# Kernel optimization log

Hardware: AMD Instinct MI355X
Metric: run time of the kernel (lower is better)

Reference implementation:

```python
import jax, jax.numpy as jnp
import numpy as np
import math

D_MODEL = 1024
NUM_HEADS = 16
D_K = D_MODEL // NUM_HEADS
B, T = 2, 2048


def setup_inputs() -> dict:
    key = jax.random.key(0)
    ks = jax.random.split(key, 9)
    s = 1.0 / math.sqrt(D_MODEL)
    inp = {
        'x': jax.random.normal(ks[0], (B, T, D_MODEL), dtype=jnp.float32),
        'mask': jnp.tril(jnp.ones((1, 1, T, T), dtype=jnp.int32)),
        'Wq': jax.random.uniform(ks[1], (D_MODEL, D_MODEL), jnp.float32, -s, s),
        'bq': jax.random.uniform(ks[2], (D_MODEL,), jnp.float32, -s, s),
        'Wk': jax.random.uniform(ks[3], (D_MODEL, D_MODEL), jnp.float32, -s, s),
        'bk': jax.random.uniform(ks[4], (D_MODEL,), jnp.float32, -s, s),
        'Wv': jax.random.uniform(ks[5], (D_MODEL, D_MODEL), jnp.float32, -s, s),
        'bv': jax.random.uniform(ks[6], (D_MODEL,), jnp.float32, -s, s),
        'Wo': jax.random.uniform(ks[7], (D_MODEL, D_MODEL), jnp.float32, -s, s),
        'bo': jax.random.uniform(ks[8], (D_MODEL,), jnp.float32, -s, s),
    }
    return inp


def reference(x, mask, Wq, bq, Wk, bk, Wv, bv, Wo, bo):
    Bsz, Tlen, C = x.shape
    # projections; torch Linear computes x @ W.T + b, here W stored as (in,out)-like square so use x @ W + b with W meaning W.T
    q = (x @ Wq + bq).reshape(Bsz, Tlen, NUM_HEADS, D_K).transpose(0, 2, 1, 3)
    k = (x @ Wk + bk).reshape(Bsz, Tlen, NUM_HEADS, D_K).transpose(0, 2, 1, 3)
    v = (x @ Wv + bv).reshape(Bsz, Tlen, NUM_HEADS, D_K).transpose(0, 2, 1, 3)
    scores = jnp.einsum('bhqd,bhkd->bhqk', q, k) / math.sqrt(D_K)  # (B,H,T,T)
    scores = jnp.where(mask == 0, -jnp.inf, scores)
    attn = jax.nn.softmax(scores, axis=-1)
    out = jnp.einsum('bhqk,bhkd->bhqd', attn, v)
    out = out.transpose(0, 2, 1, 3).reshape(Bsz, Tlen, C)
    return out @ Wo + bo
```

## Files before the change

kernel.cpp:

```cpp
#include <hip/hip_runtime.h>
#include <math.h>

typedef unsigned short ushort_t;
typedef short short8 __attribute__((ext_vector_type(8)));
typedef float f32x4 __attribute__((ext_vector_type(4)));

#define DMODEL 1024
#define NHEADS 16
#define DKH    64
#define BATCH  2
#define SEQ    2048
#define BT     (BATCH * SEQ)

__device__ __forceinline__ ushort_t f2bf(float f) {
    union { float f; unsigned u; } a; a.f = f;
    return (ushort_t)((a.u + 0x7FFFu + ((a.u >> 16) & 1u)) >> 16);
}

__device__ __forceinline__ void async_copy16(const ushort_t* g, ushort_t* l) {
    __builtin_amdgcn_global_load_lds(
        (__attribute__((address_space(1))) void*)g,
        (__attribute__((address_space(3))) void*)l, 16, 0, 0);
}

__global__ __launch_bounds__(256) void prep_kernel(
    const float* __restrict__ x, ushort_t* __restrict__ xb,
    const float* __restrict__ Wq, const float* __restrict__ Wk,
    const float* __restrict__ Wv, const float* __restrict__ Wo,
    ushort_t* __restrict__ WqT, ushort_t* __restrict__ WkT,
    ushort_t* __restrict__ WvT, ushort_t* __restrict__ WoT)
{
    __shared__ ushort_t tile[64][72];
    const int bx = blockIdx.x;
    const int tid = threadIdx.x;

    if (bx < 2048) {
        size_t i = ((size_t)bx * 256 + tid) * 8;
        float4 a = *(const float4*)(x + i);
        float4 b = *(const float4*)(x + i + 4);
        union { ushort_t u[8]; short8 v; } r;
        r.u[0] = f2bf(a.x); r.u[1] = f2bf(a.y); r.u[2] = f2bf(a.z); r.u[3] = f2bf(a.w);
        r.u[4] = f2bf(b.x); r.u[5] = f2bf(b.y); r.u[6] = f2bf(b.z); r.u[7] = f2bf(b.w);
        *(short8*)(xb + i) = r.v;
        return;
    }

    const int idx = bx - 2048;
    const int z  = idx >> 8;
    const int n0 = ((idx >> 4) & 15) * 64;
    const int k0 = (idx & 15) * 64;
    const float* W = (z == 0) ? Wq : (z == 1) ? Wk : (z == 2) ? Wv : Wo;
    ushort_t*   WT = (z == 0) ? WqT : (z == 1) ? WkT : (z == 2) ? WvT : WoT;

    const int r  = tid >> 2;
    const int cb = (tid & 3) * 16;
#pragma unroll
    for (int u = 0; u < 4; ++u) {
        float4 v = *(const float4*)(W + (size_t)(k0 + r) * DMODEL + n0 + cb + u * 4);
        union { ushort_t u4[4]; unsigned long long ll; } p;
        p.u4[0] = f2bf(v.x); p.u4[1] = f2bf(v.y); p.u4[2] = f2bf(v.z); p.u4[3] = f2bf(v.w);
        *(unsigned long long*)&tile[r][cb + u * 4] = p.ll;
    }
    __syncthreads();
    const int n  = tid >> 2;
    const int kb = (tid & 3) * 16;
#pragma unroll
    for (int half = 0; half < 2; ++half) {
        union { ushort_t u8[8]; short8 v; } p;
#pragma unroll
        for (int j = 0; j < 8; ++j) p.u8[j] = tile[kb + half * 8 + j][n];
        *(short8*)(WT + (size_t)(n0 + n) * DMODEL + k0 + kb + half * 8) = p.v;
    }
}

__device__ __forceinline__ void gemm_dbuf_128(
    const ushort_t* __restrict__ A, const ushort_t* __restrict__ B,
    int m0, int n0, ushort_t* At, ushort_t* Bt, f32x4 (&acc)[4][4])
{
    const int tid  = threadIdx.x;
    const int w    = tid >> 6, lane = tid & 63;
    const int l15  = lane & 15, quad = lane >> 4;
    const int wm   = w >> 1, wn = w & 1;
    const int srow = lane >> 3;
    const int scol = ((lane & 7) ^ srow) << 3;
    const int swz  = l15 & 7;

#pragma unroll
    for (int c = 0; c < 4; ++c) {
        int ch = w * 4 + c;
        async_copy16(A + (size_t)(m0 + ch * 8 + srow) * DMODEL + scol, At + ch * 512);
        async_copy16(B + (size_t)(n0 + ch * 8 + srow) * DMODEL + scol, Bt + ch * 512);
    }
    __syncthreads();

    for (int kt = 0; kt < DMODEL / 64; ++kt) {
        const int cur = (kt & 1) << 13;
        if (kt + 1 < DMODEL / 64) {
            const int nxt = cur ^ 8192;
            const int k0 = (kt + 1) * 64;
#pragma unroll
            for (int c = 0; c < 4; ++c) {
                int ch = w * 4 + c;
                async_copy16(A + (size_t)(m0 + ch * 8 + srow) * DMODEL + k0 + scol,
                             At + nxt + ch * 512);
                async_copy16(B + (size_t)(n0 + ch * 8 + srow) * DMODEL + k0 + scol,
                             Bt + nxt + ch * 512);
            }
        }
#pragma unroll
        for (int kk = 0; kk < 2; ++kk) {
            short8 af[4], bf[4];
#pragma unroll
            for (int t = 0; t < 4; ++t) {
                int ra = wm * 64 + t * 16 + l15;
                int rb = wn * 64 + t * 16 + l15;
                af[t] = *(const short8*)(At + cur + ra * 64 +
                                         (((kk * 4 + quad) ^ swz) << 3));
                bf[t] = *(const short8*)(Bt + cur + rb * 64 +
                                         (((kk * 4 + quad) ^ swz) << 3));
            }
#pragma unroll
            for (int mt = 0; mt < 4; ++mt)
#pragma unroll
                for (int nt = 0; nt < 4; ++nt)
                    acc[mt][nt] = __builtin_amdgcn_mfma_f32_16x16x32_bf16(
                        af[mt], bf[nt], acc[mt][nt], 0, 0, 0);
        }
        __syncthreads();
    }
}

__device__ __forceinline__ void gemm_dbuf_m64(
    const ushort_t* __restrict__ A, const ushort_t* __restrict__ B,
    int m0, int n0, ushort_t* At, ushort_t* Bt, f32x4 (&acc)[2][4])
{
    const int tid  = threadIdx.x;
    const int w    = tid >> 6, lane = tid & 63;
    const int l15  = lane & 15, quad = lane >> 4;
    const int wm   = w & 1, wn = w >> 1;
    const int srow = lane >> 3;
    const int scol = ((lane & 7) ^ srow) << 3;
    const int swz  = l15 & 7;

#pragma unroll
    for (int c = 0; c < 2; ++c) {
        int ch = w * 2 + c;
        async_copy16(A + (size_t)(m0 + ch * 8 + srow) * DMODEL + scol, At + ch * 512);
    }
#pragma unroll
    for (int c = 0; c < 4; ++c) {
        int ch = w * 4 + c;
        async_copy16(B + (size_t)(n0 + ch * 8 + srow) * DMODEL + scol, Bt + ch * 512);
    }
    __syncthreads();

    for (int kt = 0; kt < DMODEL / 64; ++kt) {
        const int curA = (kt & 1) << 12;
        const int curB = (kt & 1) << 13;
        if (kt + 1 < DMODEL / 64) {
            const int k0 = (kt + 1) * 64;
#pragma unroll
            for (int c = 0; c < 2; ++c) {
                int ch = w * 2 + c;
                async_copy16(A + (size_t)(m0 + ch * 8 + srow) * DMODEL + k0 + scol,
                             At + (curA ^ 4096) + ch * 512);
            }
#pragma unroll
            for (int c = 0; c < 4; ++c) {
                int ch = w * 4 + c;
                async_copy16(B + (size_t)(n0 + ch * 8 + srow) * DMODEL + k0 + scol,
                             Bt + (curB ^ 8192) + ch * 512);
            }
        }
#pragma unroll
        for (int kk = 0; kk < 2; ++kk) {
            short8 af[2], bf[4];
#pragma unroll
            for (int t = 0; t < 2; ++t) {
                int ra = wm * 32 + t * 16 + l15;
                af[t] = *(const short8*)(At + curA + ra * 64 +
                                         (((kk * 4 + quad) ^ swz) << 3));
            }
#pragma unroll
            for (int t = 0; t < 4; ++t) {
                int rb = wn * 64 + t * 16 + l15;
                bf[t] = *(const short8*)(Bt + curB + rb * 64 +
                                         (((kk * 4 + quad) ^ swz) << 3));
            }
#pragma unroll
            for (int mt = 0; mt < 2; ++mt)
#pragma unroll
                for (int nt = 0; nt < 4; ++nt)
                    acc[mt][nt] = __builtin_amdgcn_mfma_f32_16x16x32_bf16(
                        af[mt], bf[nt], acc[mt][nt], 0, 0, 0);
        }
        __syncthreads();
    }
}

__global__ __launch_bounds__(256) void qkv_gemm(
    const ushort_t* __restrict__ xb,
    const ushort_t* __restrict__ WqT, const ushort_t* __restrict__ WkT,
    const ushort_t* __restrict__ WvT,
    const float* __restrict__ bq, const float* __restrict__ bk,
    const float* __restrict__ bv,
    ushort_t* __restrict__ Qb, ushort_t* __restrict__ Kb, ushort_t* __restrict__ VTo)
{
    const int z = blockIdx.z;
    const ushort_t* WT = (z == 0) ? WqT : (z == 1) ? WkT : WvT;
    const float* bias  = (z == 0) ? bq : (z == 1) ? bk : bv;

    __shared__ ushort_t At[2 * 8192];
    __shared__ ushort_t Bt[2 * 8192];
    const int m0 = blockIdx.x * 128, n0 = blockIdx.y * 128;

    f32x4 zero = {0.f, 0.f, 0.f, 0.f};
    f32x4 acc[4][4];
#pragma unroll
    for (int i = 0; i < 4; ++i)
#pragma unroll
        for (int j = 0; j < 4; ++j) acc[i][j] = zero;

    gemm_dbuf_128(xb, WT, m0, n0, At, Bt, acc);

    const int tid = threadIdx.x, w = tid >> 6, lane = tid & 63;
    const int l15 = lane & 15, quad = lane >> 4;
    const int wm = w >> 1, wn = w & 1;

    float bcol[4];
#pragma unroll
    for (int nt = 0; nt < 4; ++nt) bcol[nt] = bias[n0 + wn * 64 + nt * 16 + l15];

    if (z == 2) {
#pragma unroll
        for (int mt = 0; mt < 4; ++mt) {
            int row0 = m0 + wm * 64 + mt * 16 + quad * 4;
            int b = row0 >> 11, t = row0 & (SEQ - 1);
            int tb = t & ~63;
            int idxp = ((mt & 1) << 2) | (quad << 3) | ((mt >> 1) << 5);
#pragma unroll
            for (int nt = 0; nt < 4; ++nt) {
                int col = n0 + wn * 64 + nt * 16 + l15;
                int h = col >> 6, d = col & 63;
                union { ushort_t u4[4]; unsigned long long ll; } pk;
#pragma unroll
                for (int reg = 0; reg < 4; ++reg)
                    pk.u4[reg] = f2bf(acc[mt][nt][reg] + bcol[nt]);
                *(unsigned long long*)(VTo +
                    ((size_t)(b * NHEADS + h) * DKH + d) * SEQ + tb + idxp) = pk.ll;
            }
        }
    } else {
        ushort_t* out = (z == 0) ? Qb : Kb;
#pragma unroll
        for (int mt = 0; mt < 4; ++mt)
#pragma unroll
            for (int reg = 0; reg < 4; ++reg) {
                int row = m0 + wm * 64 + mt * 16 + quad * 4 + reg;
                int b = row >> 11, t = row & (SEQ - 1);
#pragma unroll
                for (int nt = 0; nt < 4; ++nt) {
                    int col = n0 + wn * 64 + nt * 16 + l15;
                    int h = col >> 6, d = col & 63;
                    out[((((size_t)b * NHEADS + h) * SEQ + t) << 6) + d] =
                        f2bf(acc[mt][nt][reg] + bcol[nt]);
                }
            }
    }
}

__global__ __launch_bounds__(256) void attn_kernel(
    const ushort_t* __restrict__ Qb, const ushort_t* __restrict__ Kb,
    const ushort_t* __restrict__ VT, ushort_t* __restrict__ AO)
{
    const int bi = blockIdx.x;
    const int bh = bi & 31;
    const int b  = bh >> 4, h = bh & 15;
    const int qq = bi >> 5;
    const int tid = threadIdx.x, w = tid >> 6, lane = tid & 63;
    const int l15 = lane & 15, quad = lane >> 4;

    __shared__ ushort_t Kt[2][64 * 64];
    __shared__ ushort_t Vt[2][64 * 64];

    const ushort_t* Kbase = Kb + (((size_t)bh * SEQ) << 6);
    const ushort_t* Vbase = VT + (size_t)bh * DKH * SEQ;

    const int srow = lane >> 3;
    const int schx = (lane & 7) ^ srow;
    const int swz  = l15 & 7;
    const f32x4 zero = {0.f, 0.f, 0.f, 0.f};
    const float cexp = 0.18033688011112042f;

    union { ushort_t u8[8]; short8 v; } ones;
#pragma unroll
    for (int j = 0; j < 8; ++j) ones.u8[j] = 0x3F80;

    for (int job = 0; job < 2; ++job) {
        const int qt = job ? (31 - qq) : qq;
        const int q0 = qt * 64;
        const int nk = qt + 1;

        short8 qa[2];
#pragma unroll
        for (int ks = 0; ks < 2; ++ks)
            qa[ks] = *(const short8*)(
                Qb + (((size_t)bh * SEQ + q0 + w * 16 + l15) << 6) + ks * 32 + quad * 8);

        f32x4 lacc = zero;
        f32x4 o[4];
#pragma unroll
        for (int dt = 0; dt < 4; ++dt) o[dt] = zero;

#pragma unroll
        for (int c = 0; c < 2; ++c) {
            int chunk = w * 2 + c;
            async_copy16(Kbase + (((size_t)(chunk * 8 + srow)) << 6) + schx * 8,
                         &Kt[0][chunk * 512]);
            async_copy16(Vbase + (size_t)(chunk * 8 + srow) * SEQ + schx * 8,
                         &Vt[0][chunk * 512]);
        }
        __syncthreads();

        for (int kt = 0; kt < nk; ++kt) {
            const int buf = kt & 1;
            if (kt + 1 < nk) {
                const int kt0n = (kt + 1) * 64;
#pragma unroll
                for (int c = 0; c < 2; ++c) {
                    int chunk = w * 2 + c;
                    async_copy16(Kbase + (((size_t)(kt0n + chunk * 8 + srow)) << 6) + schx * 8,
                                 &Kt[buf ^ 1][chunk * 512]);
                    async_copy16(Vbase + (size_t)(chunk * 8 + srow) * SEQ + kt0n + schx * 8,
                                 &Vt[buf ^ 1][chunk * 512]);
                }
            }

            short8 kf[4][2], vf[2][4];
#pragma unroll
            for (int kt_i = 0; kt_i < 4; ++kt_i)
#pragma unroll
                for (int ks = 0; ks < 2; ++ks)
                    kf[kt_i][ks] = *(const short8*)&Kt[buf][(kt_i * 16 + l15) * 64 +
                                                            (((ks * 4 + quad) ^ swz) << 3)];
#pragma unroll
            for (int g = 0; g < 2; ++g)
#pragma unroll
                for (int dt = 0; dt < 4; ++dt)
                    vf[g][dt] = *(const short8*)&Vt[buf][(dt * 16 + l15) * 64 +
                                                         ((((g << 2) | quad) ^ swz) << 3)];

            f32x4 sc[4];
#pragma unroll
            for (int kt_i = 0; kt_i < 4; ++kt_i) sc[kt_i] = zero;
#pragma unroll
            for (int ks = 0; ks < 2; ++ks)
#pragma unroll
                for (int kt_i = 0; kt_i < 4; ++kt_i)
                    sc[kt_i] = __builtin_amdgcn_mfma_f32_16x16x32_bf16(
                        kf[kt_i][ks], qa[ks], sc[kt_i], 0, 0, 0);

            const bool domask = (kt == qt);
            const int qabs = q0 + w * 16 + l15;
            unsigned pka[4], pkb[4];
#pragma unroll
            for (int kt_i = 0; kt_i < 4; ++kt_i) {
                float p[4];
#pragma unroll
                for (int r = 0; r < 4; ++r) {
                    float pv = exp2f(cexp * sc[kt_i][r]);
                    if (domask && (kt * 64 + kt_i * 16 + quad * 4 + r) > qabs) pv = 0.f;
                    p[r] = pv;
                }
                pka[kt_i] = __builtin_amdgcn_perm(
                    __float_as_uint(p[1]), __float_as_uint(p[0]), 0x07060302u);
                pkb[kt_i] = __builtin_amdgcn_perm(
                    __float_as_uint(p[3]), __float_as_uint(p[2]), 0x07060302u);
            }

#pragma unroll
            for (int g = 0; g < 2; ++g) {
                union { unsigned u[4]; short8 v; } pf;
                pf.u[0] = pka[2 * g];
                pf.u[1] = pkb[2 * g];
                pf.u[2] = pka[2 * g + 1];
                pf.u[3] = pkb[2 * g + 1];
                lacc = __builtin_amdgcn_mfma_f32_16x16x32_bf16(
                    pf.v, ones.v, lacc, 0, 0, 0);
#pragma unroll
                for (int dt = 0; dt < 4; ++dt)
                    o[dt] = __builtin_amdgcn_mfma_f32_16x16x32_bf16(
                        pf.v, vf[g][dt], o[dt], 0, 0, 0);
            }

            __syncthreads();
        }

#pragma unroll
        for (int r = 0; r < 4; ++r) {
            float inv = 1.0f / lacc[r];
            int t = q0 + w * 16 + quad * 4 + r;
#pragma unroll
            for (int dt = 0; dt < 4; ++dt)
                AO[((size_t)b * SEQ + t) * DMODEL + h * 64 + dt * 16 + l15] =
                    f2bf(o[dt][r] * inv);
        }
    }
}

__global__ __launch_bounds__(256) void out_gemm(
    const ushort_t* __restrict__ AO, const ushort_t* __restrict__ WoT,
    const float* __restrict__ bo, float* __restrict__ out)
{
    __shared__ ushort_t At[2 * 4096];
    __shared__ ushort_t Bt[2 * 8192];
    const int m0 = blockIdx.x * 64, n0 = blockIdx.y * 128;

    f32x4 zero = {0.f, 0.f, 0.f, 0.f};
    f32x4 acc[2][4];
#pragma unroll
    for (int i = 0; i < 2; ++i)
#pragma unroll
        for (int j = 0; j < 4; ++j) acc[i][j] = zero;

    gemm_dbuf_m64(AO, WoT, m0, n0, At, Bt, acc);

    const int tid = threadIdx.x, w = tid >> 6, lane = tid & 63;
    const int l15 = lane & 15, quad = lane >> 4;
    const int wm = w & 1, wn = w >> 1;

    float bcol[4];
#pragma unroll
    for (int nt = 0; nt < 4; ++nt) bcol[nt] = bo[n0 + wn * 64 + nt * 16 + l15];

#pragma unroll
    for (int mt = 0; mt < 2; ++mt)
#pragma unroll
        for (int reg = 0; reg < 4; ++reg) {
            int row = m0 + wm * 32 + mt * 16 + quad * 4 + reg;
#pragma unroll
            for (int nt = 0; nt < 4; ++nt) {
                int col = n0 + wn * 64 + nt * 16 + l15;
                out[(size_t)row * DMODEL + col] = acc[mt][nt][reg] + bcol[nt];
            }
        }
}

extern "C" void kernel_launch(void* const* d_in, const int* in_sizes, int n_in,
                              void* d_out, int out_size, void* d_ws, size_t ws_size,
                              hipStream_t stream)
{
    const float* x  = (const float*)d_in[0];
    const float* Wq = (const float*)d_in[2];
    const float* bq = (const float*)d_in[3];
    const float* Wk = (const float*)d_in[4];
    const float* bk = (const float*)d_in[5];
    const float* Wv = (const float*)d_in[6];
    const float* bv = (const float*)d_in[7];
    const float* Wo = (const float*)d_in[8];
    const float* bo = (const float*)d_in[9];
    float* out = (float*)d_out;

    ushort_t* ws = (ushort_t*)d_ws;
    size_t off = 0;
    ushort_t* xb  = ws + off; off += (size_t)BT * DMODEL;
    ushort_t* WqT = ws + off; off += (size_t)DMODEL * DMODEL;
    ushort_t* WkT = ws + off; off += (size_t)DMODEL * DMODEL;
    ushort_t* WvT = ws + off; off += (size_t)DMODEL * DMODEL;
    ushort_t* WoT = ws + off; off += (size_t)DMODEL * DMODEL;
    ushort_t* Qb  = ws + off; off += (size_t)BT * DMODEL;
    ushort_t* Kb  = ws + off; off += (size_t)BT * DMODEL;
    ushort_t* VTb = ws + off; off += (size_t)BT * DMODEL;
    ushort_t* AOb = ws + off; off += (size_t)BT * DMODEL;

    prep_kernel<<<2048 + 1024, 256, 0, stream>>>(
        x, xb, Wq, Wk, Wv, Wo, WqT, WkT, WvT, WoT);
    qkv_gemm<<<dim3(BT / 128, DMODEL / 128, 3), 256, 0, stream>>>(
        xb, WqT, WkT, WvT, bq, bk, bv, Qb, Kb, VTb);
    attn_kernel<<<dim3(SEQ / 64 * NHEADS * BATCH / 2), 256, 0, stream>>>(
        Qb, Kb, VTb, AOb);
    out_gemm<<<dim3(BT / 64, DMODEL / 128), 256, 0, stream>>>(
        AOb, WoT, bo, out);
}
```

Baseline: 201.7 us.

## Halve GEMM K-tile to 32 with packed two-row swizzled LDS layout

Both projection GEMM helpers now stage 32-wide K slices instead of 64. Two rows are packed into each 64-element LDS line with a new XOR swizzle, and the shared buffers shrink accordingly. The goal is to cut LDS use per block so more blocks can reside on a CU and hide latency better. In exchange there are twice as many loop iterations and barriers, and each barrier covers less MFMA work.

```diff
diff --git a/kernel.cpp b/kernel.cpp
--- a/kernel.cpp
+++ b/kernel.cpp
@@ -81,51 +81,51 @@
     const int w    = tid >> 6, lane = tid & 63;
     const int l15  = lane & 15, quad = lane >> 4;
     const int wm   = w >> 1, wn = w & 1;
-    const int srow = lane >> 3;
-    const int scol = ((lane & 7) ^ srow) << 3;
-    const int swz  = l15 & 7;
-
-#pragma unroll
-    for (int c = 0; c < 4; ++c) {
-        int ch = w * 4 + c;
-        async_copy16(A + (size_t)(m0 + ch * 8 + srow) * DMODEL + scol, At + ch * 512);
-        async_copy16(B + (size_t)(n0 + ch * 8 + srow) * DMODEL + scol, Bt + ch * 512);
+    const int s    = (lane & 7) ^ ((lane >> 3) & 7);
+    const int rofs = ((lane >> 3) << 1) | (s >> 2);
+    const int cofs = (s & 3) << 3;
+
+    const ushort_t* Asrc = A + (size_t)m0 * DMODEL + cofs;
+    const ushort_t* Bsrc = B + (size_t)n0 * DMODEL + cofs;
+
+#pragma unroll
+    for (int c = 0; c < 2; ++c) {
+        int ch = w * 2 + c;
+        async_copy16(Asrc + (size_t)(ch * 16 + rofs) * DMODEL, At + ch * 512);
+        async_copy16(Bsrc + (size_t)(ch * 16 + rofs) * DMODEL, Bt + ch * 512);
     }
     __syncthreads();
 
-    for (int kt = 0; kt < DMODEL / 64; ++kt) {
-        const int cur = (kt & 1) << 13;
-        if (kt + 1 < DMODEL / 64) {
-            const int nxt = cur ^ 8192;
-            const int k0 = (kt + 1) * 64;
-#pragma unroll
-            for (int c = 0; c < 4; ++c) {
-                int ch = w * 4 + c;
-                async_copy16(A + (size_t)(m0 + ch * 8 + srow) * DMODEL + k0 + scol,
+    for (int kt = 0; kt < DMODEL / 32; ++kt) {
+        const int cur = (kt & 1) << 12;
+        if (kt + 1 < DMODEL / 32) {
+            const int nxt = cur ^ 4096;
+            const int k0 = (kt + 1) * 32;
+#pragma unroll
+            for (int c = 0; c < 2; ++c) {
+                int ch = w * 2 + c;
+                async_copy16(Asrc + (size_t)(ch * 16 + rofs) * DMODEL + k0,
                              At + nxt + ch * 512);
-                async_copy16(B + (size_t)(n0 + ch * 8 + srow) * DMODEL + k0 + scol,
+                async_copy16(Bsrc + (size_t)(ch * 16 + rofs) * DMODEL + k0,
                              Bt + nxt + ch * 512);
             }
         }
-#pragma unroll
-        for (int kk = 0; kk < 2; ++kk) {
-            short8 af[4], bf[4];
-#pragma unroll
-            for (int t = 0; t < 4; ++t) {
-                int ra = wm * 64 + t * 16 + l15;
-                int rb = wn * 64 + t * 16 + l15;
-                af[t] = *(const short8*)(At + cur + ra * 64 +
-                                         (((kk * 4 + quad) ^ swz) << 3));
-                bf[t] = *(const short8*)(Bt + cur + rb * 64 +
-                                         (((kk * 4 + quad) ^ swz) << 3));
-            }
-#pragma unroll
-            for (int mt = 0; mt < 4; ++mt)
-#pragma unroll
-                for (int nt = 0; nt < 4; ++nt)
-                    acc[mt][nt] = __builtin_amdgcn_mfma_f32_16x16x32_bf16(
-                        af[mt], bf[nt], acc[mt][nt], 0, 0, 0);
-        }
+        short8 af[4], bf[4];
+#pragma unroll
+        for (int t = 0; t < 4; ++t) {
+            int ra = wm * 64 + t * 16 + l15;
+            int rb = wn * 64 + t * 16 + l15;
+            af[t] = *(const short8*)(At + cur + (ra >> 1) * 64 +
+                     (((((ra & 1) << 2) | quad) ^ ((ra >> 1) & 7)) << 3));
+            bf[t] = *(const short8*)(Bt + cur + (rb >> 1) * 64 +
+                     (((((rb & 1) << 2) | quad) ^ ((rb >> 1) & 7)) << 3));
+        }
+#pragma unroll
+        for (int mt = 0; mt < 4; ++mt)
+#pragma unroll
+            for (int nt = 0; nt < 4; ++nt)
+                acc[mt][nt] = __builtin_amdgcn_mfma_f32_16x16x32_bf16(
+                    af[mt], bf[nt], acc[mt][nt], 0, 0, 0);
         __syncthreads();
     }
 }
@@ -138,62 +138,54 @@
     const int w    = tid >> 6, lane = tid & 63;
     const int l15  = lane & 15, quad = lane >> 4;
     const int wm   = w & 1, wn = w >> 1;
-    const int srow = lane >> 3;
-    const int scol = ((lane & 7) ^ srow) << 3;
-    const int swz  = l15 & 7;
-
+    const int s    = (lane & 7) ^ ((lane >> 3) & 7);
+    const int rofs = ((lane >> 3) << 1) | (s >> 2);
+    const int cofs = (s & 3) << 3;
+
+    const ushort_t* Asrc = A + (size_t)m0 * DMODEL + cofs;
+    const ushort_t* Bsrc = B + (size_t)n0 * DMODEL + cofs;
+
+    async_copy16(Asrc + (size_t)(w * 16 + rofs) * DMODEL, At + w * 512);
 #pragma unroll
     for (int c = 0; c < 2; ++c) {
         int ch = w * 2 + c;
-        async_copy16(A + (size_t)(m0 + ch * 8 + srow) * DMODEL + scol, At + ch * 512);
-    }
-#pragma unroll
-    for (int c = 0; c < 4; ++c) {
-        int ch = w * 4 + c;
-        async_copy16(B + (size_t)(n0 + ch * 8 + srow) * DMODEL + scol, Bt + ch * 512);
+        async_copy16(Bsrc + (size_t)(ch * 16 + rofs) * DMODEL, Bt + ch * 512);
     }
     __syncthreads();
 
-    for (int kt = 0; kt < DMODEL / 64; ++kt) {
-        const int curA = (kt & 1) << 12;
-        const int curB = (kt & 1) << 13;
-        if (kt + 1 < DMODEL / 64) {
-            const int k0 = (kt + 1) * 64;
+    for (int kt = 0; kt < DMODEL / 32; ++kt) {
+        const int curA = (kt & 1) << 11;
+        const int curB = (kt & 1) << 12;
+        if (kt + 1 < DMODEL / 32) {
+            const int k0 = (kt + 1) * 32;
+            async_copy16(Asrc + (size_t)(w * 16 + rofs) * DMODEL + k0,
+                         At + (curA ^ 2048) + w * 512);
 #pragma unroll
             for (int c = 0; c < 2; ++c) {
                 int ch = w * 2 + c;
-                async_copy16(A + (size_t)(m0 + ch * 8 + srow) * DMODEL + k0 + scol,
-                             At + (curA ^ 4096) + ch * 512);
-            }
-#pragma unroll
-            for (int c = 0; c < 4; ++c) {
-                int ch = w * 4 + c;
-                async_copy16(B + (size_t)(n0 + ch * 8 + srow) * DMODEL + k0 + scol,
-                             Bt + (curB ^ 8192) + ch * 512);
-            }
-        }
-#pragma unroll
-        for (int kk = 0; kk < 2; ++kk) {
-            short8 af[2], bf[4];
-#pragma unroll
-            for (int t = 0; t < 2; ++t) {
-                int ra = wm * 32 + t * 16 + l15;
-                af[t] = *(const short8*)(At + curA + ra * 64 +
-                                         (((kk * 4 + quad) ^ swz) << 3));
-            }
-#pragma unroll
-            for (int t = 0; t < 4; ++t) {
-                int rb = wn * 64 + t * 16 + l15;
-                bf[t] = *(const short8*)(Bt + curB + rb * 64 +
-                                         (((kk * 4 + quad) ^ swz) << 3));
-            }
-#pragma unroll
-            for (int mt = 0; mt < 2; ++mt)
-#pragma unroll
-                for (int nt = 0; nt < 4; ++nt)
-                    acc[mt][nt] = __builtin_amdgcn_mfma_f32_16x16x32_bf16(
-                        af[mt], bf[nt], acc[mt][nt], 0, 0, 0);
-        }
+                async_copy16(Bsrc + (size_t)(ch * 16 + rofs) * DMODEL + k0,
+                             Bt + (curB ^ 4096) + ch * 512);
+            }
+        }
+        short8 af[2], bf[4];
+#pragma unroll
+        for (int t = 0; t < 2; ++t) {
+            int ra = wm * 32 + t * 16 + l15;
+            af[t] = *(const short8*)(At + curA + (ra >> 1) * 64 +
+                     (((((ra & 1) << 2) | quad) ^ ((ra >> 1) & 7)) << 3));
+        }
+#pragma unroll
+        for (int t = 0; t < 4; ++t) {
+            int rb = wn * 64 + t * 16 + l15;
+            bf[t] = *(const short8*)(Bt + curB + (rb >> 1) * 64 +
+                     (((((rb & 1) << 2) | quad) ^ ((rb >> 1) & 7)) << 3));
+        }
+#pragma unroll
+        for (int mt = 0; mt < 2; ++mt)
+#pragma unroll
+            for (int nt = 0; nt < 4; ++nt)
+                acc[mt][nt] = __builtin_amdgcn_mfma_f32_16x16x32_bf16(
+                    af[mt], bf[nt], acc[mt][nt], 0, 0, 0);
         __syncthreads();
     }
 }
@@ -210,8 +202,8 @@
     const ushort_t* WT = (z == 0) ? WqT : (z == 1) ? WkT : WvT;
     const float* bias  = (z == 0) ? bq : (z == 1) ? bk : bv;
 
-    __shared__ ushort_t At[2 * 8192];
-    __shared__ ushort_t Bt[2 * 8192];
+    __shared__ ushort_t At[2 * 4096];
+    __shared__ ushort_t Bt[2 * 4096];
     const int m0 = blockIdx.x * 128, n0 = blockIdx.y * 128;
 
     f32x4 zero = {0.f, 0.f, 0.f, 0.f};
@@ -412,8 +404,8 @@
     const ushort_t* __restrict__ AO, const ushort_t* __restrict__ WoT,
     const float* __restrict__ bo, float* __restrict__ out)
 {
-    __shared__ ushort_t At[2 * 4096];
-    __shared__ ushort_t Bt[2 * 8192];
+    __shared__ ushort_t At[2 * 2048];
+    __shared__ ushort_t Bt[2 * 4096];
     const int m0 = blockIdx.x * 64, n0 = blockIdx.y * 128;
 
     f32x4 zero = {0.f, 0.f, 0.f, 0.f};
```

After: 211.4 us. +4.8%, slower.

## Fuse all stages into one persistent kernel with software grid barriers

Applied to the files above, without the earlier changes.

Replaces the four separate launches (prep, QKV GEMM, attention, output GEMM) with a single persistent kernel of 768 blocks that loops over work items and uses atomic-counter grid barriers between stages. The QKV GEMM now uses a 32-wide K step with a new swizzled LDS layout so shared memory fits three blocks per CU, and the stages share memory through a union. This removes launch gaps and tail effects between kernels, but adds spin-wait barrier cost, depends on all 768 blocks being co-resident, and fixes the grid size per stage.

```diff
diff --git a/kernel.cpp b/kernel.cpp
--- a/kernel.cpp
+++ b/kernel.cpp
@@ -11,6 +11,7 @@
 #define BATCH  2
 #define SEQ    2048
 #define BT     (BATCH * SEQ)
+#define NBLK   768
 
 __device__ __forceinline__ ushort_t f2bf(float f) {
     union { float f; unsigned u; } a; a.f = f;
@@ -23,101 +24,139 @@
         (__attribute__((address_space(3))) void*)l, 16, 0, 0);
 }
 
-__global__ __launch_bounds__(256) void prep_kernel(
-    const float* __restrict__ x, ushort_t* __restrict__ xb,
-    const float* __restrict__ Wq, const float* __restrict__ Wk,
-    const float* __restrict__ Wv, const float* __restrict__ Wo,
-    ushort_t* __restrict__ WqT, ushort_t* __restrict__ WkT,
-    ushort_t* __restrict__ WvT, ushort_t* __restrict__ WoT)
-{
-    __shared__ ushort_t tile[64][72];
-    const int bx = blockIdx.x;
-    const int tid = threadIdx.x;
-
-    if (bx < 2048) {
-        size_t i = ((size_t)bx * 256 + tid) * 8;
-        float4 a = *(const float4*)(x + i);
-        float4 b = *(const float4*)(x + i + 4);
-        union { ushort_t u[8]; short8 v; } r;
-        r.u[0] = f2bf(a.x); r.u[1] = f2bf(a.y); r.u[2] = f2bf(a.z); r.u[3] = f2bf(a.w);
-        r.u[4] = f2bf(b.x); r.u[5] = f2bf(b.y); r.u[6] = f2bf(b.z); r.u[7] = f2bf(b.w);
-        *(short8*)(xb + i) = r.v;
-        return;
-    }
-
-    const int idx = bx - 2048;
-    const int z  = idx >> 8;
-    const int n0 = ((idx >> 4) & 15) * 64;
-    const int k0 = (idx & 15) * 64;
-    const float* W = (z == 0) ? Wq : (z == 1) ? Wk : (z == 2) ? Wv : Wo;
-    ushort_t*   WT = (z == 0) ? WqT : (z == 1) ? WkT : (z == 2) ? WvT : WoT;
-
-    const int r  = tid >> 2;
-    const int cb = (tid & 3) * 16;
-#pragma unroll
-    for (int u = 0; u < 4; ++u) {
-        float4 v = *(const float4*)(W + (size_t)(k0 + r) * DMODEL + n0 + cb + u * 4);
-        union { ushort_t u4[4]; unsigned long long ll; } p;
-        p.u4[0] = f2bf(v.x); p.u4[1] = f2bf(v.y); p.u4[2] = f2bf(v.z); p.u4[3] = f2bf(v.w);
-        *(unsigned long long*)&tile[r][cb + u * 4] = p.ll;
+__device__ __forceinline__ void grid_barrier(unsigned* cnt) {
+    __syncthreads();
+    if (threadIdx.x == 0) {
+        __threadfence();
+        __hip_atomic_fetch_add(cnt, 1u, __ATOMIC_ACQ_REL, __HIP_MEMORY_SCOPE_AGENT);
+        while (__hip_atomic_load(cnt, __ATOMIC_ACQUIRE, __HIP_MEMORY_SCOPE_AGENT) < NBLK)
+            __builtin_amdgcn_s_sleep(1);
     }
     __syncthreads();
-    const int n  = tid >> 2;
-    const int kb = (tid & 3) * 16;
-#pragma unroll
-    for (int half = 0; half < 2; ++half) {
-        union { ushort_t u8[8]; short8 v; } p;
-#pragma unroll
-        for (int j = 0; j < 8; ++j) p.u8[j] = tile[kb + half * 8 + j][n];
-        *(short8*)(WT + (size_t)(n0 + n) * DMODEL + k0 + kb + half * 8) = p.v;
-    }
 }
 
-__device__ __forceinline__ void gemm_dbuf_128(
-    const ushort_t* __restrict__ A, const ushort_t* __restrict__ B,
-    int m0, int n0, ushort_t* At, ushort_t* Bt, f32x4 (&acc)[4][4])
+union Shm {
+    struct { ushort_t At[2 * 4096]; ushort_t Bt[2 * 4096]; } q;
+    struct { ushort_t At[2 * 4096]; ushort_t Bt[2 * 8192]; } o;
+    struct { ushort_t Kt[2][4096]; ushort_t Vt[2][4096]; } a;
+    ushort_t tile[64][72];
+};
+
+__global__ __launch_bounds__(256, 3) void fused_kernel(
+    const float* __restrict__ x,
+    const float* __restrict__ Wq, const float* __restrict__ bq,
+    const float* __restrict__ Wk, const float* __restrict__ bk,
+    const float* __restrict__ Wv, const float* __restrict__ bv,
+    const float* __restrict__ Wo, const float* __restrict__ bo,
+    ushort_t* __restrict__ xb,
+    ushort_t* __restrict__ WqT, ushort_t* __restrict__ WkT,
+    ushort_t* __restrict__ WvT, ushort_t* __restrict__ WoT,
+    ushort_t* __restrict__ Qb, ushort_t* __restrict__ Kb,
+    ushort_t* __restrict__ VTb, ushort_t* __restrict__ AOb,
+    float* __restrict__ out, unsigned* __restrict__ bar)
 {
-    const int tid  = threadIdx.x;
+    __shared__ Shm sh;
+    const int bx  = blockIdx.x;
+    const int tid = threadIdx.x;
     const int w    = tid >> 6, lane = tid & 63;
     const int l15  = lane & 15, quad = lane >> 4;
-    const int wm   = w >> 1, wn = w & 1;
-    const int srow = lane >> 3;
-    const int scol = ((lane & 7) ^ srow) << 3;
-    const int swz  = l15 & 7;
-
-#pragma unroll
-    for (int c = 0; c < 4; ++c) {
-        int ch = w * 4 + c;
-        async_copy16(A + (size_t)(m0 + ch * 8 + srow) * DMODEL + scol, At + ch * 512);
-        async_copy16(B + (size_t)(n0 + ch * 8 + srow) * DMODEL + scol, Bt + ch * 512);
+    const f32x4 zero = {0.f, 0.f, 0.f, 0.f};
+
+    for (int j = bx; j < 3072; j += NBLK) {
+        if (j < 2048) {
+            size_t i = ((size_t)j * 256 + tid) * 8;
+            float4 a = *(const float4*)(x + i);
+            float4 b = *(const float4*)(x + i + 4);
+            union { ushort_t u[8]; short8 v; } r;
+            r.u[0] = f2bf(a.x); r.u[1] = f2bf(a.y); r.u[2] = f2bf(a.z); r.u[3] = f2bf(a.w);
+            r.u[4] = f2bf(b.x); r.u[5] = f2bf(b.y); r.u[6] = f2bf(b.z); r.u[7] = f2bf(b.w);
+            *(short8*)(xb + i) = r.v;
+        } else {
+            const int idx = j - 2048;
+            const int z  = idx >> 8;
+            const int n0 = ((idx >> 4) & 15) * 64;
+            const int k0 = (idx & 15) * 64;
+            const float* W = (z == 0) ? Wq : (z == 1) ? Wk : (z == 2) ? Wv : Wo;
+            ushort_t*   WT = (z == 0) ? WqT : (z == 1) ? WkT : (z == 2) ? WvT : WoT;
+
+            const int r  = tid >> 2;
+            const int cb = (tid & 3) * 16;
+#pragma unroll
+            for (int u = 0; u < 4; ++u) {
+                float4 v = *(const float4*)(W + (size_t)(k0 + r) * DMODEL + n0 + cb + u * 4);
+                union { ushort_t u4[4]; unsigned long long ll; } p;
+                p.u4[0] = f2bf(v.x); p.u4[1] = f2bf(v.y);
+                p.u4[2] = f2bf(v.z); p.u4[3] = f2bf(v.w);
+                *(unsigned long long*)&sh.tile[r][cb + u * 4] = p.ll;
+            }
+            __syncthreads();
+            const int n  = tid >> 2;
+            const int kb = (tid & 3) * 16;
+#pragma unroll
+            for (int half = 0; half < 2; ++half) {
+                union { ushort_t u8[8]; short8 v; } p;
+#pragma unroll
+                for (int jj = 0; jj < 8; ++jj) p.u8[jj] = sh.tile[kb + half * 8 + jj][n];
+                *(short8*)(WT + (size_t)(n0 + n) * DMODEL + k0 + kb + half * 8) = p.v;
+            }
+            __syncthreads();
+        }
     }
-    __syncthreads();
-
-    for (int kt = 0; kt < DMODEL / 64; ++kt) {
-        const int cur = (kt & 1) << 13;
-        if (kt + 1 < DMODEL / 64) {
-            const int nxt = cur ^ 8192;
-            const int k0 = (kt + 1) * 64;
-#pragma unroll
-            for (int c = 0; c < 4; ++c) {
-                int ch = w * 4 + c;
-                async_copy16(A + (size_t)(m0 + ch * 8 + srow) * DMODEL + k0 + scol,
-                             At + nxt + ch * 512);
-                async_copy16(B + (size_t)(n0 + ch * 8 + srow) * DMODEL + k0 + scol,
-                             Bt + nxt + ch * 512);
-            }
-        }
-#pragma unroll
-        for (int kk = 0; kk < 2; ++kk) {
+
+    grid_barrier(&bar[0]);
+
+    {
+        const int z   = bx >> 8;
+        const int rem = bx & 255;
+        const int m0  = (rem & 31) * 128, n0 = (rem >> 5) * 128;
+        const ushort_t* WT = (z == 0) ? WqT : (z == 1) ? WkT : WvT;
+        const float* bias  = (z == 0) ? bq : (z == 1) ? bk : bv;
+
+        const int wm = w >> 1, wn = w & 1;
+        const int s    = (lane & 7) ^ ((lane >> 3) & 7);
+        const int rofs = ((lane >> 3) << 1) | (s >> 2);
+        const int cofs = (s & 3) << 3;
+
+        f32x4 acc[4][4];
+#pragma unroll
+        for (int i = 0; i < 4; ++i)
+#pragma unroll
+            for (int jj = 0; jj < 4; ++jj) acc[i][jj] = zero;
+
+        const ushort_t* Asrc = xb + (size_t)m0 * DMODEL + cofs;
+        const ushort_t* Bsrc = WT + (size_t)n0 * DMODEL + cofs;
+
+#pragma unroll
+        for (int c = 0; c < 2; ++c) {
+            int ch = w * 2 + c;
+            async_copy16(Asrc + (size_t)(ch * 16 + rofs) * DMODEL, sh.q.At + ch * 512);
+            async_copy16(Bsrc + (size_t)(ch * 16 + rofs) * DMODEL, sh.q.Bt + ch * 512);
+        }
+        __syncthreads();
+
+        for (int kt = 0; kt < DMODEL / 32; ++kt) {
+            const int cur = (kt & 1) << 12;
+            if (kt + 1 < DMODEL / 32) {
+                const int nxt = cur ^ 4096;
+                const int k0 = (kt + 1) * 32;
+#pragma unroll
+                for (int c = 0; c < 2; ++c) {
+                    int ch = w * 2 + c;
+                    async_copy16(Asrc + (size_t)(ch * 16 + rofs) * DMODEL + k0,
+                                 sh.q.At + nxt + ch * 512);
+                    async_copy16(Bsrc + (size_t)(ch * 16 + rofs) * DMODEL + k0,
+                                 sh.q.Bt + nxt + ch * 512);
+                }
+            }
             short8 af[4], bf[4];
 #pragma unroll
             for (int t = 0; t < 4; ++t) {
                 int ra = wm * 64 + t * 16 + l15;
                 int rb = wn * 64 + t * 16 + l15;
-                af[t] = *(const short8*)(At + cur + ra * 64 +
-                                         (((kk * 4 + quad) ^ swz) << 3));
-                bf[t] = *(const short8*)(Bt + cur + rb * 64 +
-                                         (((kk * 4 + quad) ^ swz) << 3));
+                af[t] = *(const short8*)(sh.q.At + cur + (ra >> 1) * 64 +
+                         (((((ra & 1) << 2) | quad) ^ ((ra >> 1) & 7)) << 3));
+                bf[t] = *(const short8*)(sh.q.Bt + cur + (rb >> 1) * 64 +
+                         (((((rb & 1) << 2) | quad) ^ ((rb >> 1) & 7)) << 3));
             }
 #pragma unroll
             for (int mt = 0; mt < 4; ++mt)
@@ -125,325 +164,271 @@
                 for (int nt = 0; nt < 4; ++nt)
                     acc[mt][nt] = __builtin_amdgcn_mfma_f32_16x16x32_bf16(
                         af[mt], bf[nt], acc[mt][nt], 0, 0, 0);
-        }
-        __syncthreads();
-    }
-}
-
-__device__ __forceinline__ void gemm_dbuf_m64(
-    const ushort_t* __restrict__ A, const ushort_t* __restrict__ B,
-    int m0, int n0, ushort_t* At, ushort_t* Bt, f32x4 (&acc)[2][4])
-{
-    const int tid  = threadIdx.x;
-    const int w    = tid >> 6, lane = tid & 63;
-    const int l15  = lane & 15, quad = lane >> 4;
-    const int wm   = w & 1, wn = w >> 1;
-    const int srow = lane >> 3;
-    const int scol = ((lane & 7) ^ srow) << 3;
-    const int swz  = l15 & 7;
-
-#pragma unroll
-    for (int c = 0; c < 2; ++c) {
-        int ch = w * 2 + c;
-        async_copy16(A + (size_t)(m0 + ch * 8 + srow) * DMODEL + scol, At + ch * 512);
-    }
-#pragma unroll
-    for (int c = 0; c < 4; ++c) {
-        int ch = w * 4 + c;
-        async_copy16(B + (size_t)(n0 + ch * 8 + srow) * DMODEL + scol, Bt + ch * 512);
-    }
-    __syncthreads();
-
-    for (int kt = 0; kt < DMODEL / 64; ++kt) {
-        const int curA = (kt & 1) << 12;
-        const int curB = (kt & 1) << 13;
-        if (kt + 1 < DMODEL / 64) {
-            const int k0 = (kt + 1) * 64;
-#pragma unroll
-            for (int c = 0; c < 2; ++c) {
-                int ch = w * 2 + c;
-                async_copy16(A + (size_t)(m0 + ch * 8 + srow) * DMODEL + k0 + scol,
-                             At + (curA ^ 4096) + ch * 512);
-            }
-#pragma unroll
-            for (int c = 0; c < 4; ++c) {
-                int ch = w * 4 + c;
-                async_copy16(B + (size_t)(n0 + ch * 8 + srow) * DMODEL + k0 + scol,
-                             Bt + (curB ^ 8192) + ch * 512);
-            }
-        }
-#pragma unroll
-        for (int kk = 0; kk < 2; ++kk) {
-            short8 af[2], bf[4];
-#pragma unroll
-            for (int t = 0; t < 2; ++t) {
-                int ra = wm * 32 + t * 16 + l15;
-                af[t] = *(const short8*)(At + curA + ra * 64 +
-                                         (((kk * 4 + quad) ^ swz) << 3));
-            }
-#pragma unroll
-            for (int t = 0; t < 4; ++t) {
-                int rb = wn * 64 + t * 16 + l15;
-                bf[t] = *(const short8*)(Bt + curB + rb * 64 +
-                                         (((kk * 4 + quad) ^ swz) << 3));
-            }
-#pragma unroll
-            for (int mt = 0; mt < 2; ++mt)
-#pragma unroll
-                for (int nt = 0; nt < 4; ++nt)
-                    acc[mt][nt] = __builtin_amdgcn_mfma_f32_16x16x32_bf16(
-                        af[mt], bf[nt], acc[mt][nt], 0, 0, 0);
-        }
-        __syncthreads();
-    }
-}
-
-__global__ __launch_bounds__(256) void qkv_gemm(
-    const ushort_t* __restrict__ xb,
-    const ushort_t* __restrict__ WqT, const ushort_t* __restrict__ WkT,
-    const ushort_t* __restrict__ WvT,
-    const float* __restrict__ bq, const float* __restrict__ bk,
-    const float* __restrict__ bv,
-    ushort_t* __restrict__ Qb, ushort_t* __restrict__ Kb, ushort_t* __restrict__ VTo)
-{
-    const int z = blockIdx.z;
-    const ushort_t* WT = (z == 0) ? WqT : (z == 1) ? WkT : WvT;
-    const float* bias  = (z == 0) ? bq : (z == 1) ? bk : bv;
-
-    __shared__ ushort_t At[2 * 8192];
-    __shared__ ushort_t Bt[2 * 8192];
-    const int m0 = blockIdx.x * 128, n0 = blockIdx.y * 128;
-
-    f32x4 zero = {0.f, 0.f, 0.f, 0.f};
-    f32x4 acc[4][4];
-#pragma unroll
-    for (int i = 0; i < 4; ++i)
-#pragma unroll
-        for (int j = 0; j < 4; ++j) acc[i][j] = zero;
-
-    gemm_dbuf_128(xb, WT, m0, n0, At, Bt, acc);
-
-    const int tid = threadIdx.x, w = tid >> 6, lane = tid & 63;
-    const int l15 = lane & 15, quad = lane >> 4;
-    const int wm = w >> 1, wn = w & 1;
-
-    float bcol[4];
-#pragma unroll
-    for (int nt = 0; nt < 4; ++nt) bcol[nt] = bias[n0 + wn * 64 + nt * 16 + l15];
-
-    if (z == 2) {
-#pragma unroll
-        for (int mt = 0; mt < 4; ++mt) {
-            int row0 = m0 + wm * 64 + mt * 16 + quad * 4;
-            int b = row0 >> 11, t = row0 & (SEQ - 1);
-            int tb = t & ~63;
-            int idxp = ((mt & 1) << 2) | (quad << 3) | ((mt >> 1) << 5);
-#pragma unroll
-            for (int nt = 0; nt < 4; ++nt) {
-                int col = n0 + wn * 64 + nt * 16 + l15;
-                int h = col >> 6, d = col & 63;
-                union { ushort_t u4[4]; unsigned long long ll; } pk;
-#pragma unroll
-                for (int reg = 0; reg < 4; ++reg)
-                    pk.u4[reg] = f2bf(acc[mt][nt][reg] + bcol[nt]);
-                *(unsigned long long*)(VTo +
-                    ((size_t)(b * NHEADS + h) * DKH + d) * SEQ + tb + idxp) = pk.ll;
-            }
-        }
-    } else {
-        ushort_t* out = (z == 0) ? Qb : Kb;
-#pragma unroll
-        for (int mt = 0; mt < 4; ++mt)
-#pragma unroll
-            for (int reg = 0; reg < 4; ++reg) {
-                int row = m0 + wm * 64 + mt * 16 + quad * 4 + reg;
-                int b = row >> 11, t = row & (SEQ - 1);
+            __syncthreads();
+        }
+
+        float bcol[4];
+#pragma unroll
+        for (int nt = 0; nt < 4; ++nt) bcol[nt] = bias[n0 + wn * 64 + nt * 16 + l15];
+
+        if (z == 2) {
+#pragma unroll
+            for (int mt = 0; mt < 4; ++mt) {
+                int row0 = m0 + wm * 64 + mt * 16 + quad * 4;
+                int b = row0 >> 11, t = row0 & (SEQ - 1);
+                int tb = t & ~63;
+                int idxp = ((mt & 1) << 2) | (quad << 3) | ((mt >> 1) << 5);
 #pragma unroll
                 for (int nt = 0; nt < 4; ++nt) {
                     int col = n0 + wn * 64 + nt * 16 + l15;
                     int h = col >> 6, d = col & 63;
-                    out[((((size_t)b * NHEADS + h) * SEQ + t) << 6) + d] =
-                        f2bf(acc[mt][nt][reg] + bcol[nt]);
-                }
-            }
+                    union { ushort_t u4[4]; unsigned long long ll; } pk;
+#pragma unroll
+                    for (int reg = 0; reg < 4; ++reg)
+                        pk.u4[reg] = f2bf(acc[mt][nt][reg] + bcol[nt]);
+                    *(unsigned long long*)(VTb +
+                        ((size_t)(b * NHEADS + h) * DKH + d) * SEQ + tb + idxp) = pk.ll;
+                }
+            }
+        } else {
+            ushort_t* outp = (z == 0) ? Qb : Kb;
+#pragma unroll
+            for (int mt = 0; mt < 4; ++mt)
+#pragma unroll
+                for (int reg = 0; reg < 4; ++reg) {
+                    int row = m0 + wm * 64 + mt * 16 + quad * 4 + reg;
+                    int b = row >> 11, t = row & (SEQ - 1);
+#pragma unroll
+                    for (int nt = 0; nt < 4; ++nt) {
+                        int col = n0 + wn * 64 + nt * 16 + l15;
+                        int h = col >> 6, d = col & 63;
+                        outp[((((size_t)b * NHEADS + h) * SEQ + t) << 6) + d] =
+                            f2bf(acc[mt][nt][reg] + bcol[nt]);
+                    }
+                }
+        }
     }
-}
-
-__global__ __launch_bounds__(256) void attn_kernel(
-    const ushort_t* __restrict__ Qb, const ushort_t* __restrict__ Kb,
-    const ushort_t* __restrict__ VT, ushort_t* __restrict__ AO)
-{
-    const int bi = blockIdx.x;
-    const int bh = bi & 31;
-    const int b  = bh >> 4, h = bh & 15;
-    const int qq = bi >> 5;
-    const int tid = threadIdx.x, w = tid >> 6, lane = tid & 63;
-    const int l15 = lane & 15, quad = lane >> 4;
-
-    __shared__ ushort_t Kt[2][64 * 64];
-    __shared__ ushort_t Vt[2][64 * 64];
-
-    const ushort_t* Kbase = Kb + (((size_t)bh * SEQ) << 6);
-    const ushort_t* Vbase = VT + (size_t)bh * DKH * SEQ;
-
-    const int srow = lane >> 3;
-    const int schx = (lane & 7) ^ srow;
-    const int swz  = l15 & 7;
-    const f32x4 zero = {0.f, 0.f, 0.f, 0.f};
-    const float cexp = 0.18033688011112042f;
-
-    union { ushort_t u8[8]; short8 v; } ones;
-#pragma unroll
-    for (int j = 0; j < 8; ++j) ones.u8[j] = 0x3F80;
-
-    for (int job = 0; job < 2; ++job) {
-        const int qt = job ? (31 - qq) : qq;
-        const int q0 = qt * 64;
-        const int nk = qt + 1;
-
-        short8 qa[2];
-#pragma unroll
-        for (int ks = 0; ks < 2; ++ks)
-            qa[ks] = *(const short8*)(
-                Qb + (((size_t)bh * SEQ + q0 + w * 16 + l15) << 6) + ks * 32 + quad * 8);
-
-        f32x4 lacc = zero;
-        f32x4 o[4];
-#pragma unroll
-        for (int dt = 0; dt < 4; ++dt) o[dt] = zero;
+
+    grid_barrier(&bar[1]);
+
+    if (bx < 512) {
+        const int bi = bx;
+        const int bh = bi & 31;
+        const int b  = bh >> 4, h = bh & 15;
+        const int qq = bi >> 5;
+
+        const ushort_t* Kbase = Kb + (((size_t)bh * SEQ) << 6);
+        const ushort_t* Vbase = VTb + (size_t)bh * DKH * SEQ;
+
+        const int srow = lane >> 3;
+        const int schx = (lane & 7) ^ srow;
+        const int swz  = l15 & 7;
+        const float cexp = 0.18033688011112042f;
+
+        union { ushort_t u8[8]; short8 v; } ones;
+#pragma unroll
+        for (int jj = 0; jj < 8; ++jj) ones.u8[jj] = 0x3F80;
+
+        for (int job = 0; job < 2; ++job) {
+            const int qt = job ? (31 - qq) : qq;
+            const int q0 = qt * 64;
+            const int nk = qt + 1;
+
+            short8 qa[2];
+#pragma unroll
+            for (int ks = 0; ks < 2; ++ks)
+                qa[ks] = *(const short8*)(
+                    Qb + (((size_t)bh * SEQ + q0 + w * 16 + l15) << 6) + ks * 32 + quad * 8);
+
+            f32x4 lacc = zero;
+            f32x4 o[4];
+#pragma unroll
+            for (int dt = 0; dt < 4; ++dt) o[dt] = zero;
+
+#pragma unroll
+            for (int c = 0; c < 2; ++c) {
+                int chunk = w * 2 + c;
+                async_copy16(Kbase + (((size_t)(chunk * 8 + srow)) << 6) + schx * 8,
+                             &sh.a.Kt[0][chunk * 512]);
+                async_copy16(Vbase + (size_t)(chunk * 8 + srow) * SEQ + schx * 8,
+                             &sh.a.Vt[0][chunk * 512]);
+            }
+            __syncthreads();
+
+            for (int kt = 0; kt < nk; ++kt) {
+                const int buf = kt & 1;
+                if (kt + 1 < nk) {
+                    const int kt0n = (kt + 1) * 64;
+#pragma unroll
+                    for (int c = 0; c < 2; ++c) {
+                        int chunk = w * 2 + c;
+                        async_copy16(Kbase + (((size_t)(kt0n + chunk * 8 + srow)) << 6) + schx * 8,
+                                     &sh.a.Kt[buf ^ 1][chunk * 512]);
+                        async_copy16(Vbase + (size_t)(chunk * 8 + srow) * SEQ + kt0n + schx * 8,
+                                     &sh.a.Vt[buf ^ 1][chunk * 512]);
+                    }
+                }
+
+                short8 kf[4][2], vf[2][4];
+#pragma unroll
+                for (int kt_i = 0; kt_i < 4; ++kt_i)
+#pragma unroll
+                    for (int ks = 0; ks < 2; ++ks)
+                        kf[kt_i][ks] = *(const short8*)&sh.a.Kt[buf][(kt_i * 16 + l15) * 64 +
+                                                        (((ks * 4 + quad) ^ swz) << 3)];
+#pragma unroll
+                for (int g = 0; g < 2; ++g)
+#pragma unroll
+                    for (int dt = 0; dt < 4; ++dt)
+                        vf[g][dt] = *(const short8*)&sh.a.Vt[buf][(dt * 16 + l15) * 64 +
+                                                     ((((g << 2) | quad) ^ swz) << 3)];
+
+                f32x4 sc[4];
+#pragma unroll
+                for (int kt_i = 0; kt_i < 4; ++kt_i) sc[kt_i] = zero;
+#pragma unroll
+                for (int ks = 0; ks < 2; ++ks)
+#pragma unroll
+                    for (int kt_i = 0; kt_i < 4; ++kt_i)
+                        sc[kt_i] = __builtin_amdgcn_mfma_f32_16x16x32_bf16(
+                            kf[kt_i][ks], qa[ks], sc[kt_i], 0, 0, 0);
+
+                const bool domask = (kt == qt);
+                const int qabs = q0 + w * 16 + l15;
+                unsigned pka[4], pkb[4];
+#pragma unroll
+                for (int kt_i = 0; kt_i < 4; ++kt_i) {
+                    float p[4];
+#pragma unroll
+                    for (int r = 0; r < 4; ++r) {
+                        float pv = exp2f(cexp * sc[kt_i][r]);
+                        if (domask && (kt * 64 + kt_i * 16 + quad * 4 + r) > qabs) pv = 0.f;
+                        p[r] = pv;
+                    }
+                    pka[kt_i] = __builtin_amdgcn_perm(
+                        __float_as_uint(p[1]), __float_as_uint(p[0]), 0x07060302u);
+                    pkb[kt_i] = __builtin_amdgcn_perm(
+                        __float_as_uint(p[3]), __float_as_uint(p[2]), 0x07060302u);
+                }
+
+#pragma unroll
+                for (int g = 0; g < 2; ++g) {
+                    union { unsigned u[4]; short8 v; } pf;
+                    pf.u[0] = pka[2 * g];
+                    pf.u[1] = pkb[2 * g];
+                    pf.u[2] = pka[2 * g + 1];
+                    pf.u[3] = pkb[2 * g + 1];
+                    lacc = __builtin_amdgcn_mfma_f32_16x16x32_bf16(
+                        pf.v, ones.v, lacc, 0, 0, 0);
+#pragma unroll
+                    for (int dt = 0; dt < 4; ++dt)
+                        o[dt] = __builtin_amdgcn_mfma_f32_16x16x32_bf16(
+                            pf.v, vf[g][dt], o[dt], 0, 0, 0);
+                }
+
+                __syncthreads();
+            }
+
+#pragma unroll
+            for (int r = 0; r < 4; ++r) {
+                float inv = 1.0f / lacc[r];
+                int t = q0 + w * 16 + quad * 4 + r;
+#pragma unroll
+                for (int dt = 0; dt < 4; ++dt)
+                    AOb[((size_t)b * SEQ + t) * DMODEL + h * 64 + dt * 16 + l15] =
+                        f2bf(o[dt][r] * inv);
+            }
+        }
+    }
+
+    grid_barrier(&bar[2]);
+
+    if (bx < 512) {
+        const int m0 = (bx & 63) * 64, n0 = (bx >> 6) * 128;
+        const int wm = w & 1, wn = w >> 1;
+        const int srow = lane >> 3;
+        const int scol = ((lane & 7) ^ srow) << 3;
+        const int swz  = l15 & 7;
+
+        f32x4 acc[2][4];
+#pragma unroll
+        for (int i = 0; i < 2; ++i)
+#pragma unroll
+            for (int jj = 0; jj < 4; ++jj) acc[i][jj] = zero;
 
 #pragma unroll
         for (int c = 0; c < 2; ++c) {
-            int chunk = w * 2 + c;
-            async_copy16(Kbase + (((size_t)(chunk * 8 + srow)) << 6) + schx * 8,
-                         &Kt[0][chunk * 512]);
-            async_copy16(Vbase + (size_t)(chunk * 8 + srow) * SEQ + schx * 8,
-                         &Vt[0][chunk * 512]);
+            int ch = w * 2 + c;
+            async_copy16(AOb + (size_t)(m0 + ch * 8 + srow) * DMODEL + scol,
+                         sh.o.At + ch * 512);
+        }
+#pragma unroll
+        for (int c = 0; c < 4; ++c) {
+            int ch = w * 4 + c;
+            async_copy16(WoT + (size_t)(n0 + ch * 8 + srow) * DMODEL + scol,
+                         sh.o.Bt + ch * 512);
         }
         __syncthreads();
 
-        for (int kt = 0; kt < nk; ++kt) {
-            const int buf = kt & 1;
-            if (kt + 1 < nk) {
-                const int kt0n = (kt + 1) * 64;
+        for (int kt = 0; kt < DMODEL / 64; ++kt) {
+            const int curA = (kt & 1) << 12;
+            const int curB = (kt & 1) << 13;
+            if (kt + 1 < DMODEL / 64) {
+                const int k0 = (kt + 1) * 64;
 #pragma unroll
                 for (int c = 0; c < 2; ++c) {
-                    int chunk = w * 2 + c;
-                    async_copy16(Kbase + (((size_t)(kt0n + chunk * 8 + srow)) << 6) + schx * 8,
-                                 &Kt[buf ^ 1][chunk * 512]);
-                    async_copy16(Vbase + (size_t)(chunk * 8 + srow) * SEQ + kt0n + schx * 8,
-                                 &Vt[buf ^ 1][chunk * 512]);
-                }
-            }
-
-            short8 kf[4][2], vf[2][4];
-#pragma unroll
-            for (int kt_i = 0; kt_i < 4; ++kt_i)
-#pragma unroll
-                for (int ks = 0; ks < 2; ++ks)
-                    kf[kt_i][ks] = *(const short8*)&Kt[buf][(kt_i * 16 + l15) * 64 +
-                                                            (((ks * 4 + quad) ^ swz) << 3)];
-#pragma unroll
-            for (int g = 0; g < 2; ++g)
-#pragma unroll
-                for (int dt = 0; dt < 4; ++dt)
-                    vf[g][dt] = *(const short8*)&Vt[buf][(dt * 16 + l15) * 64 +
-                                                         ((((g << 2) | quad) ^ swz) << 3)];
-
-            f32x4 sc[4];
-#pragma unroll
-            for (int kt_i = 0; kt_i < 4; ++kt_i) sc[kt_i] = zero;
-#pragma unroll
-            for (int ks = 0; ks < 2; ++ks)
-#pragma unroll
-                for (int kt_i = 0; kt_i < 4; ++kt_i)
-                    sc[kt_i] = __builtin_amdgcn_mfma_f32_16x16x32_bf16(
-                        kf[kt_i][ks], qa[ks], sc[kt_i], 0, 0, 0);
-
-            const bool domask = (kt == qt);
-            const int qabs = q0 + w * 16 + l15;
-            unsigned pka[4], pkb[4];
-#pragma unroll
-            for (int kt_i = 0; kt_i < 4; ++kt_i) {
-                float p[4];
-#pragma unroll
-                for (int r = 0; r < 4; ++r) {
-                    float pv = exp2f(cexp * sc[kt_i][r]);
-                    if (domask && (kt * 64 + kt_i * 16 + quad * 4 + r) > qabs) pv = 0.f;
-                    p[r] = pv;
-                }
-                pka[kt_i] = __builtin_amdgcn_perm(
-                    __float_as_uint(p[1]), __float_as_uint(p[0]), 0x07060302u);
-                pkb[kt_i] = __builtin_amdgcn_perm(
-                    __float_as_uint(p[3]), __float_as_uint(p[2]), 0x07060302u);
-            }
-
-#pragma unroll
-            for (int g = 0; g < 2; ++g) {
-                union { unsigned u[4]; short8 v; } pf;
-                pf.u[0] = pka[2 * g];
-                pf.u[1] = pkb[2 * g];
-                pf.u[2] = pka[2 * g + 1];
-                pf.u[3] = pkb[2 * g + 1];
-                lacc = __builtin_amdgcn_mfma_f32_16x16x32_bf16(
-                    pf.v, ones.v, lacc, 0, 0, 0);
-#pragma unroll
-                for (int dt = 0; dt < 4; ++dt)
-                    o[dt] = __builtin_amdgcn_mfma_f32_16x16x32_bf16(
-                        pf.v, vf[g][dt], o[dt], 0, 0, 0);
-            }
-
+                    int ch = w * 2 + c;
+                    async_copy16(AOb + (size_t)(m0 + ch * 8 + srow) * DMODEL + k0 + scol,
+                                 sh.o.At + (curA ^ 4096) + ch * 512);
+                }
+#pragma unroll
+                for (int c = 0; c < 4; ++c) {
+                    int ch = w * 4 + c;
+                    async_copy16(WoT + (size_t)(n0 + ch * 8 + srow) * DMODEL + k0 + scol,
+                                 sh.o.Bt + (curB ^ 8192) + ch * 512);
+                }
+            }
+#pragma unroll
+            for (int kk = 0; kk < 2; ++kk) {
+                short8 af[2], bf[4];
+#pragma unroll
+                for (int t = 0; t < 2; ++t) {
+                    int ra = wm * 32 + t * 16 + l15;
+                    af[t] = *(const short8*)(sh.o.At + curA + ra * 64 +
+                                             (((kk * 4 + quad) ^ swz) << 3));
+                }
+#pragma unroll
+                for (int t = 0; t < 4; ++t) {
+                    int rb = wn * 64 + t * 16 + l15;
+                    bf[t] = *(const short8*)(sh.o.Bt + curB + rb * 64 +
+                                             (((kk * 4 + quad) ^ swz) << 3));
+                }
+#pragma unroll
+                for (int mt = 0; mt < 2; ++mt)
+#pragma unroll
+                    for (int nt = 0; nt < 4; ++nt)
+                        acc[mt][nt] = __builtin_amdgcn_mfma_f32_16x16x32_bf16(
+                            af[mt], bf[nt], acc[mt][nt], 0, 0, 0);
+            }
             __syncthreads();
         }
 
-#pragma unroll
-        for (int r = 0; r < 4; ++r) {
-            float inv = 1.0f / lacc[r];
-            int t = q0 + w * 16 + quad * 4 + r;
-#pragma unroll
-            for (int dt = 0; dt < 4; ++dt)
-                AO[((size_t)b * SEQ + t) * DMODEL + h * 64 + dt * 16 + l15] =
-                    f2bf(o[dt][r] * inv);
-        }
+        float bcol[4];
+#pragma unroll
+        for (int nt = 0; nt < 4; ++nt) bcol[nt] = bo[n0 + wn * 64 + nt * 16 + l15];
+
+#pragma unroll
+        for (int mt = 0; mt < 2; ++mt)
+#pragma unroll
+            for (int reg = 0; reg < 4; ++reg) {
+                int row = m0 + wm * 32 + mt * 16 + quad * 4 + reg;
+#pragma unroll
+                for (int nt = 0; nt < 4; ++nt) {
+                    int col = n0 + wn * 64 + nt * 16 + l15;
+                    out[(size_t)row * DMODEL + col] = acc[mt][nt][reg] + bcol[nt];
+                }
+            }
     }
-}
-
-__global__ __launch_bounds__(256) void out_gemm(
-    const ushort_t* __restrict__ AO, const ushort_t* __restrict__ WoT,
-    const float* __restrict__ bo, float* __restrict__ out)
-{
-    __shared__ ushort_t At[2 * 4096];
-    __shared__ ushort_t Bt[2 * 8192];
-    const int m0 = blockIdx.x * 64, n0 = blockIdx.y * 128;
-
-    f32x4 zero = {0.f, 0.f, 0.f, 0.f};
-    f32x4 acc[2][4];
-#pragma unroll
-    for (int i = 0; i < 2; ++i)
-#pragma unroll
-        for (int j = 0; j < 4; ++j) acc[i][j] = zero;
-
-    gemm_dbuf_m64(AO, WoT, m0, n0, At, Bt, acc);
-
-    const int tid = threadIdx.x, w = tid >> 6, lane = tid & 63;
-    const int l15 = lane & 15, quad = lane >> 4;
-    const int wm = w & 1, wn = w >> 1;
-
-    float bcol[4];
-#pragma unroll
-    for (int nt = 0; nt < 4; ++nt) bcol[nt] = bo[n0 + wn * 64 + nt * 16 + l15];
-
-#pragma unroll
-    for (int mt = 0; mt < 2; ++mt)
-#pragma unroll
-        for (int reg = 0; reg < 4; ++reg) {
-            int row = m0 + wm * 32 + mt * 16 + quad * 4 + reg;
-#pragma unroll
-            for (int nt = 0; nt < 4; ++nt) {
-                int col = n0 + wn * 64 + nt * 16 + l15;
-                out[(size_t)row * DMODEL + col] = acc[mt][nt][reg] + bcol[nt];
-            }
-        }
 }
 
 extern "C" void kernel_launch(void* const* d_in, const int* in_sizes, int n_in,
@@ -472,13 +457,10 @@
     ushort_t* Kb  = ws + off; off += (size_t)BT * DMODEL;
     ushort_t* VTb = ws + off; off += (size_t)BT * DMODEL;
     ushort_t* AOb = ws + off; off += (size_t)BT * DMODEL;
-
-    prep_kernel<<<2048 + 1024, 256, 0, stream>>>(
-        x, xb, Wq, Wk, Wv, Wo, WqT, WkT, WvT, WoT);
-    qkv_gemm<<<dim3(BT / 128, DMODEL / 128, 3), 256, 0, stream>>>(
-        xb, WqT, WkT, WvT, bq, bk, bv, Qb, Kb, VTb);
-    attn_kernel<<<dim3(SEQ / 64 * NHEADS * BATCH / 2), 256, 0, stream>>>(
-        Qb, Kb, VTb, AOb);
-    out_gemm<<<dim3(BT / 64, DMODEL / 128), 256, 0, stream>>>(
-        AOb, WoT, bo, out);
+    unsigned* bar = (unsigned*)(ws + off);
+
+    hipMemsetAsync(bar, 0, 64, stream);
+    fused_kernel<<<NBLK, 256, 0, stream>>>(
+        x, Wq, bq, Wk, bk, Wv, bv, Wo, bo,
+        xb, WqT, WkT, WvT, WoT, Qb, Kb, VTb, AOb, out, bar);
 }
```

Result: slower. 549.6 us (+172.4%).
